# Optimization experiments

Hardware: AMD Instinct MI355X
Metric: run time of the kernel (lower is better)

Reference implementation:

```python
import jax, jax.numpy as jnp
import numpy as np

N = 500_000
D = 256
D_OUT = 256
B = 16_384


def setup_inputs() -> dict:
    key = jax.random.key(0)
    ks = jax.random.split(key, 10)
    x = jax.random.normal(ks[0], (N, D), dtype=jnp.float32)
    batch = jnp.sort(jax.random.randint(ks[1], (N,), 0, B))
    last_click_mask = jax.random.uniform(ks[2], (N,), dtype=jnp.float32)
    s = 1.0 / np.sqrt(D)
    W1 = jax.random.uniform(ks[3], (D, D), jnp.float32, -s, s)
    b1 = jax.random.uniform(ks[4], (D,), jnp.float32, -s, s)
    W2 = jax.random.uniform(ks[5], (D, D), jnp.float32, -s, s)
    b2 = jax.random.uniform(ks[6], (D,), jnp.float32, -s, s)
    w3 = jax.random.uniform(ks[7], (D, 1), jnp.float32, -s, s)
    s4 = 1.0 / np.sqrt(2 * D)
    W4 = jax.random.uniform(ks[8], (2 * D, D_OUT), jnp.float32, -s4, s4)
    b4 = jax.random.uniform(ks[9], (D_OUT,), jnp.float32, -s4, s4)
    return {
        "x": x,
        "batch": batch,
        "last_click_mask": last_click_mask,
        "num_segments": B,
        "W1": W1, "b1": b1, "W2": W2, "b2": b2,
        "w3": w3, "W4": W4, "b4": b4,
    }


def reference(x, batch, last_click_mask, num_segments, W1, b1, W2, b2, w3, W4, b4):
    # local_rep = global_add_pool(x * mask, batch)  -> [B, D]
    local_rep = jax.ops.segment_sum(x * last_click_mask[:, None], batch,
                                    num_segments=num_segments)
    local_rep_repeat = local_rep[batch]                       # [N, D] gather
    att = jax.nn.sigmoid(local_rep_repeat @ W1 + b1 + x @ W2 + b2) @ w3  # [N, 1]
    weighted_x = x * att                                      # [N, D]
    global_rep = jax.ops.segment_sum(weighted_x, batch,
                                     num_segments=num_segments)  # [B, D]
    rep = jnp.concatenate([local_rep, global_rep], axis=1)    # [B, 2D]
    return rep @ W4 + b4                                      # [B, D_OUT]
```

## Files before the change

kernel.cpp:

```cpp
#include <hip/hip_runtime.h>
#include <hip/hip_bf16.h>

#define NROWS 500000
#define DIM   256
#define BSEG  16384
#define LDSP  264

typedef __attribute__((ext_vector_type(8))) short short8;
typedef __attribute__((ext_vector_type(4))) float floatx4;


__device__ __forceinline__ unsigned short f2bf(float f) {
  unsigned u = __float_as_uint(f);
  unsigned r = u + 0x7fffu + ((u >> 16) & 1u);
  return (unsigned short)(r >> 16);
}
__device__ __forceinline__ float bf2f(short s) {
  return __uint_as_float(((unsigned)(unsigned short)s) << 16);
}
__device__ __forceinline__ float fast_sigmoid(float z) {
  return 1.0f / (1.0f + __expf(-z));
}

__global__ __launch_bounds__(1024) void k_zero(float* __restrict__ p, int n4) {
  int i = blockIdx.x * blockDim.x + threadIdx.x;
  if (i < n4) ((float4*)p)[i] = make_float4(0.f, 0.f, 0.f, 0.f);
}

__global__ __launch_bounds__(256) void k_convert_wt(
    const float* __restrict__ W, short* __restrict__ out, int K)
{
  int idx = blockIdx.x * blockDim.x + threadIdx.x;
  int kt = idx >> 8, n = idx & 255;
  if (kt * 32 >= K) return;
  short tmp[32];
#pragma unroll
  for (int kk = 0; kk < 32; ++kk)
    tmp[kk] = (short)f2bf(W[(size_t)(kt * 32 + kk) * DIM + n]);
#pragma unroll
  for (int kk = 0; kk < 32; kk += 4)
    *(short4*)&out[(size_t)idx * 32 + kk] = *(short4*)&tmp[kk];
}

__global__ __launch_bounds__(256) void k_seg_local(
    const float* __restrict__ x, const int* __restrict__ batch,
    const float* __restrict__ mask, float* __restrict__ local_rep,
    int rows_per_block)
{
  const int col = threadIdx.x;
  int r0 = blockIdx.x * rows_per_block;
  int r1 = min(NROWS, r0 + rows_per_block);
  if (r0 >= r1) return;
  float acc = 0.f;
  int cur = batch[r0];
  int r = r0;
  for (; r + 4 <= r1; r += 4) {
    float xv0 = x[(size_t)(r + 0) * DIM + col];
    float xv1 = x[(size_t)(r + 1) * DIM + col];
    float xv2 = x[(size_t)(r + 2) * DIM + col];
    float xv3 = x[(size_t)(r + 3) * DIM + col];
    int s0 = batch[r], s1 = batch[r + 1], s2 = batch[r + 2], s3 = batch[r + 3];
    float m0 = mask[r], m1 = mask[r + 1], m2 = mask[r + 2], m3 = mask[r + 3];
    if (s0 != cur) { atomicAdd(&local_rep[(size_t)cur * DIM + col], acc); acc = 0.f; cur = s0; }
    acc = fmaf(xv0, m0, acc);
    if (s1 != cur) { atomicAdd(&local_rep[(size_t)cur * DIM + col], acc); acc = 0.f; cur = s1; }
    acc = fmaf(xv1, m1, acc);
    if (s2 != cur) { atomicAdd(&local_rep[(size_t)cur * DIM + col], acc); acc = 0.f; cur = s2; }
    acc = fmaf(xv2, m2, acc);
    if (s3 != cur) { atomicAdd(&local_rep[(size_t)cur * DIM + col], acc); acc = 0.f; cur = s3; }
    acc = fmaf(xv3, m3, acc);
  }
  for (; r < r1; ++r) {
    int s = batch[r];
    float xv = x[(size_t)r * DIM + col];
    float mv = mask[r];
    if (s != cur) { atomicAdd(&local_rep[(size_t)cur * DIM + col], acc); acc = 0.f; cur = s; }
    acc = fmaf(xv, mv, acc);
  }
  atomicAdd(&local_rep[(size_t)cur * DIM + col], acc);
}

__device__ __forceinline__ void stage_tile(const float* __restrict__ A, int row0,
                                           int maxrow, short* xs, int tid)
{
#pragma unroll
  for (int it = 0; it < 16; ++it) {
    int linear = it * 256 + tid;
    int r = linear >> 6;
    int c4 = linear & 63;
    int row = min(row0 + r, maxrow);
    float4 v = *(const float4*)&A[(size_t)row * DIM + c4 * 4];
    short4 o;
    o.x = (short)f2bf(v.x); o.y = (short)f2bf(v.y);
    o.z = (short)f2bf(v.z); o.w = (short)f2bf(v.w);
    *(short4*)&xs[r * LDSP + c4 * 4] = o;
  }
}

__device__ __forceinline__ void mfma_pass(const short* xs, const short* __restrict__ Wt,
                                          floatx4 acc[4][4], int lane15, int quad, int n0)
{
  for (int kt = 0; kt < 8; ++kt) {
    short8 bfr[4], afr[4];
#pragma unroll
    for (int jn = 0; jn < 4; ++jn)
      bfr[jn] = *(const short8*)&Wt[(size_t)kt * 8192 + (n0 + jn * 16 + lane15) * 32 + quad * 8];
#pragma unroll
    for (int i = 0; i < 4; ++i)
      afr[i] = *(const short8*)&xs[(i * 16 + lane15) * LDSP + kt * 32 + quad * 8];
#pragma unroll
    for (int i = 0; i < 4; ++i)
#pragma unroll
      for (int jn = 0; jn < 4; ++jn)
        acc[i][jn] = __builtin_amdgcn_mfma_f32_16x16x32_bf16(afr[i], bfr[jn], acc[i][jn], 0, 0, 0);
  }
}

__global__ __launch_bounds__(256) void k_h1_mfma(
    const float* __restrict__ A, const short* __restrict__ Wt,
    const float* __restrict__ bias, short* __restrict__ H1bf)
{
  __shared__ short xs[64 * LDSP];
  const int tid = threadIdx.x;
  const int row0 = blockIdx.x * 64;
  stage_tile(A, row0, BSEG - 1, xs, tid);
  __syncthreads();
  const int lane = tid & 63, wave = tid >> 6;
  const int lane15 = lane & 15, quad = lane >> 4;
  const int n0 = wave * 64;
  floatx4 acc[4][4];
#pragma unroll
  for (int i = 0; i < 4; ++i)
#pragma unroll
    for (int j = 0; j < 4; ++j) acc[i][j] = (floatx4)0.f;
  mfma_pass(xs, Wt, acc, lane15, quad, n0);
#pragma unroll
  for (int i = 0; i < 4; ++i)
#pragma unroll
    for (int jn = 0; jn < 4; ++jn) {
      int col = n0 + jn * 16 + lane15;
      float bv = bias[col];
#pragma unroll
      for (int r = 0; r < 4; ++r) {
        int row = row0 + i * 16 + quad * 4 + r;
        H1bf[(size_t)row * DIM + col] = (short)f2bf(acc[i][jn][r] + bv);
      }
    }
}

__global__ __launch_bounds__(256) void k_fused_main(
    const float* __restrict__ x, const int* __restrict__ batch,
    const short* __restrict__ W2t, const float* __restrict__ b2,
    const float* __restrict__ w3, const short* __restrict__ H1bf,
    float* __restrict__ global_rep)
{
  __shared__ short xs[64 * LDSP];
  __shared__ int   seg_s[64];
  __shared__ float att_s[64];
  const int tid = threadIdx.x;
  const int row0 = blockIdx.x * 64;

  stage_tile(x, row0, NROWS - 1, xs, tid);
  if (tid < 64) {
    seg_s[tid] = batch[min(row0 + tid, NROWS - 1)];
    att_s[tid] = 0.f;
  }
  __syncthreads();

  const int lane = tid & 63, wave = tid >> 6;
  const int lane15 = lane & 15, quad = lane >> 4;
  const int n0 = wave * 64;
  floatx4 acc[4][4];
#pragma unroll
  for (int i = 0; i < 4; ++i)
#pragma unroll
    for (int j = 0; j < 4; ++j) acc[i][j] = (floatx4)0.f;
  mfma_pass(xs, W2t, acc, lane15, quad, n0);

  float b2v[4], w3v[4];
#pragma unroll
  for (int jn = 0; jn < 4; ++jn) {
    int col = n0 + jn * 16 + lane15;
    b2v[jn] = b2[col];
    w3v[jn] = w3[col];
  }
  float part[4][4];
#pragma unroll
  for (int i = 0; i < 4; ++i)
#pragma unroll
    for (int r = 0; r < 4; ++r) {
      int rl = i * 16 + quad * 4 + r;
      int seg = seg_s[rl];
      float p = 0.f;
#pragma unroll
      for (int jn = 0; jn < 4; ++jn) {
        int col = n0 + jn * 16 + lane15;
        float h = bf2f(H1bf[(size_t)seg * DIM + col]);
        float z = acc[i][jn][r] + h + b2v[jn];
        p = fmaf(fast_sigmoid(z), w3v[jn], p);
      }
      part[i][r] = p;
    }
#pragma unroll
  for (int off = 1; off < 16; off <<= 1)
#pragma unroll
    for (int i = 0; i < 4; ++i)
#pragma unroll
      for (int r = 0; r < 4; ++r)
        part[i][r] += __shfl_xor(part[i][r], off, 64);
  if (lane15 == 0) {
#pragma unroll
    for (int i = 0; i < 4; ++i)
#pragma unroll
      for (int r = 0; r < 4; ++r)
        atomicAdd(&att_s[i * 16 + quad * 4 + r], part[i][r]);
  }
  __syncthreads();

  const int col = tid;
  const int rmax = min(64, NROWS - row0);
  float acc2 = 0.f;
  int cur = seg_s[0];
  for (int r = 0; r < rmax; ++r) {
    int s = seg_s[r];
    float xv = bf2f(xs[r * LDSP + col]);
    float av = att_s[r];
    if (s != cur) {
      atomicAdd(&global_rep[(size_t)cur * DIM + col], acc2);
      acc2 = 0.f; cur = s;
    }
    acc2 = fmaf(xv, av, acc2);
  }
  atomicAdd(&global_rep[(size_t)cur * DIM + col], acc2);
}

__global__ __launch_bounds__(256) void k_out_mfma(
    const float* __restrict__ local_rep, const float* __restrict__ global_rep,
    const short* __restrict__ W4t, const float* __restrict__ b4,
    float* __restrict__ out)
{
  __shared__ short xs[64 * LDSP];
  const int tid = threadIdx.x;
  const int row0 = blockIdx.x * 64;
  const int lane = tid & 63, wave = tid >> 6;
  const int lane15 = lane & 15, quad = lane >> 4;
  const int n0 = wave * 64;
  floatx4 acc[4][4];
#pragma unroll
  for (int i = 0; i < 4; ++i)
#pragma unroll
    for (int j = 0; j < 4; ++j) acc[i][j] = (floatx4)0.f;

  stage_tile(local_rep, row0, BSEG - 1, xs, tid);
  __syncthreads();
  mfma_pass(xs, W4t, acc, lane15, quad, n0);
  __syncthreads();
  stage_tile(global_rep, row0, BSEG - 1, xs, tid);
  __syncthreads();
  mfma_pass(xs, W4t + (size_t)8 * 8192, acc, lane15, quad, n0);

#pragma unroll
  for (int i = 0; i < 4; ++i)
#pragma unroll
    for (int jn = 0; jn < 4; ++jn) {
      int col = n0 + jn * 16 + lane15;
      float bv = b4[col];
#pragma unroll
      for (int r = 0; r < 4; ++r) {
        int row = row0 + i * 16 + quad * 4 + r;
        out[(size_t)row * DIM + col] = acc[i][jn][r] + bv;
      }
    }
}

extern "C" void kernel_launch(void* const* d_in, const int* in_sizes, int n_in,
                              void* d_out, int out_size, void* d_ws, size_t ws_size,
                              hipStream_t stream) {
  (void)in_sizes; (void)n_in; (void)out_size; (void)ws_size;
  const float* x    = (const float*)d_in[0];
  const int*   batch= (const int*)d_in[1];
  const float* mask = (const float*)d_in[2];
  const float* W1 = (const float*)d_in[4];
  const float* b1 = (const float*)d_in[5];
  const float* W2 = (const float*)d_in[6];
  const float* b2 = (const float*)d_in[7];
  const float* w3 = (const float*)d_in[8];
  const float* W4 = (const float*)d_in[9];
  const float* b4 = (const float*)d_in[10];
  float* out = (float*)d_out;

  char* base = (char*)d_ws;
  float* local_rep  = (float*)(base);
  float* global_rep = (float*)(base + (size_t)16 * 1024 * 1024);
  short* H1bf       = (short*)(base + (size_t)32 * 1024 * 1024);
  short* W1t        = (short*)(base + (size_t)40 * 1024 * 1024);
  short* W2t        = (short*)(base + (size_t)40 * 1024 * 1024 + 128 * 1024);
  short* W4t        = (short*)(base + (size_t)40 * 1024 * 1024 + 256 * 1024);

  int n4 = 2 * BSEG * DIM / 4;
  hipLaunchKernelGGL(k_zero, dim3(n4 / 1024), dim3(1024), 0, stream, local_rep, n4);

  hipLaunchKernelGGL(k_convert_wt, dim3(8),  dim3(256), 0, stream, W1, W1t, 256);
  hipLaunchKernelGGL(k_convert_wt, dim3(8),  dim3(256), 0, stream, W2, W2t, 256);
  hipLaunchKernelGGL(k_convert_wt, dim3(16), dim3(256), 0, stream, W4, W4t, 512);

  const int SEG_BLOCKS = 2048;
  int rpb = (NROWS + SEG_BLOCKS - 1) / SEG_BLOCKS;
  hipLaunchKernelGGL(k_seg_local, dim3(SEG_BLOCKS), dim3(256), 0, stream,
                     x, batch, mask, local_rep, rpb);

  hipLaunchKernelGGL(k_h1_mfma, dim3(BSEG / 64), dim3(256), 0, stream,
                     local_rep, W1t, b1, H1bf);

  hipLaunchKernelGGL(k_fused_main, dim3((NROWS + 63) / 64), dim3(256), 0, stream,
                     x, batch, W2t, b2, w3, H1bf, global_rep);

  hipLaunchKernelGGL(k_out_mfma, dim3(BSEG / 64), dim3(256), 0, stream,
                     local_rep, global_rep, W4t, b4, out);
}
```

Before: 991.1 us.

## Merge weight conversions, double-buffer MFMA fragments, double segment-sum blocks

Folds the three weight-conversion launches into one 32-block kernel, removing two launch overheads. Adds register double-buffering in the MFMA inner loop so the next k-tile's A and B fragments load while the current tile's MFMAs issue. Doubles the block count for the local segment-sum kernel to raise parallelism. The prefetch raises register pressure, and more segment blocks mean more boundary atomics.

After: 1.023 ms. +3.2%, slower.

```diff
diff --git a/kernel.cpp b/kernel.cpp
--- a/kernel.cpp
+++ b/kernel.cpp
@@ -27,19 +27,25 @@
   if (i < n4) ((float4*)p)[i] = make_float4(0.f, 0.f, 0.f, 0.f);
 }
 
-__global__ __launch_bounds__(256) void k_convert_wt(
-    const float* __restrict__ W, short* __restrict__ out, int K)
-{
-  int idx = blockIdx.x * blockDim.x + threadIdx.x;
-  int kt = idx >> 8, n = idx & 255;
-  if (kt * 32 >= K) return;
+__global__ __launch_bounds__(256) void k_convert_all(
+    const float* __restrict__ W1, const float* __restrict__ W2,
+    const float* __restrict__ W4, short* __restrict__ W1t,
+    short* __restrict__ W2t, short* __restrict__ W4t)
+{
+  int blk = blockIdx.x;
+  const float* W; short* out; int kt;
+  if (blk < 8)       { W = W1; out = W1t; kt = blk; }
+  else if (blk < 16) { W = W2; out = W2t; kt = blk - 8; }
+  else               { W = W4; out = W4t; kt = blk - 16; }
+  int n = threadIdx.x;
   short tmp[32];
 #pragma unroll
   for (int kk = 0; kk < 32; ++kk)
     tmp[kk] = (short)f2bf(W[(size_t)(kt * 32 + kk) * DIM + n]);
+  size_t base = ((size_t)kt * 256 + n) * 32;
 #pragma unroll
   for (int kk = 0; kk < 32; kk += 4)
-    *(short4*)&out[(size_t)idx * 32 + kk] = *(short4*)&tmp[kk];
+    *(short4*)&out[base + kk] = *(short4*)&tmp[kk];
 }
 
 __global__ __launch_bounds__(256) void k_seg_local(
@@ -100,19 +106,31 @@
 __device__ __forceinline__ void mfma_pass(const short* xs, const short* __restrict__ Wt,
                                           floatx4 acc[4][4], int lane15, int quad, int n0)
 {
+  short8 bfr[2][4], afr[2][4];
+#pragma unroll
+  for (int jn = 0; jn < 4; ++jn)
+    bfr[0][jn] = *(const short8*)&Wt[(size_t)(n0 + jn * 16 + lane15) * 32 + quad * 8];
+#pragma unroll
+  for (int i = 0; i < 4; ++i)
+    afr[0][i] = *(const short8*)&xs[(i * 16 + lane15) * LDSP + quad * 8];
+
+#pragma unroll
   for (int kt = 0; kt < 8; ++kt) {
-    short8 bfr[4], afr[4];
-#pragma unroll
-    for (int jn = 0; jn < 4; ++jn)
-      bfr[jn] = *(const short8*)&Wt[(size_t)kt * 8192 + (n0 + jn * 16 + lane15) * 32 + quad * 8];
+    const int cur = kt & 1, nxt = cur ^ 1;
+    if (kt < 7) {
+      const int k2 = kt + 1;
+#pragma unroll
+      for (int jn = 0; jn < 4; ++jn)
+        bfr[nxt][jn] = *(const short8*)&Wt[(size_t)k2 * 8192 + (n0 + jn * 16 + lane15) * 32 + quad * 8];
+#pragma unroll
+      for (int i = 0; i < 4; ++i)
+        afr[nxt][i] = *(const short8*)&xs[(i * 16 + lane15) * LDSP + k2 * 32 + quad * 8];
+    }
 #pragma unroll
     for (int i = 0; i < 4; ++i)
-      afr[i] = *(const short8*)&xs[(i * 16 + lane15) * LDSP + kt * 32 + quad * 8];
-#pragma unroll
-    for (int i = 0; i < 4; ++i)
 #pragma unroll
       for (int jn = 0; jn < 4; ++jn)
-        acc[i][jn] = __builtin_amdgcn_mfma_f32_16x16x32_bf16(afr[i], bfr[jn], acc[i][jn], 0, 0, 0);
+        acc[i][jn] = __builtin_amdgcn_mfma_f32_16x16x32_bf16(afr[cur][i], bfr[cur][jn], acc[i][jn], 0, 0, 0);
   }
 }
 
@@ -300,11 +318,10 @@
   int n4 = 2 * BSEG * DIM / 4;
   hipLaunchKernelGGL(k_zero, dim3(n4 / 1024), dim3(1024), 0, stream, local_rep, n4);
 
-  hipLaunchKernelGGL(k_convert_wt, dim3(8),  dim3(256), 0, stream, W1, W1t, 256);
-  hipLaunchKernelGGL(k_convert_wt, dim3(8),  dim3(256), 0, stream, W2, W2t, 256);
-  hipLaunchKernelGGL(k_convert_wt, dim3(16), dim3(256), 0, stream, W4, W4t, 512);
-
-  const int SEG_BLOCKS = 2048;
+  hipLaunchKernelGGL(k_convert_all, dim3(32), dim3(256), 0, stream,
+                     W1, W2, W4, W1t, W2t, W4t);
+
+  const int SEG_BLOCKS = 4096;
   int rpb = (NROWS + SEG_BLOCKS - 1) / SEG_BLOCKS;
   hipLaunchKernelGGL(k_seg_local, dim3(SEG_BLOCKS), dim3(256), 0, stream,
                      x, batch, mask, local_rep, rpb);
```
